# Performance work log

Measured on AMD Instinct MI355X. Metric: run time of the kernel, lower is better.

## Reference

```python
import jax, jax.numpy as jnp
import numpy as np

EPS = 1e-4  # scn BatchNormalization default eps
N, K, C = 500000, 9, 64  # active sites, kernel offsets (1x3x3), channels


def setup_inputs() -> dict:
    key = jax.random.key(0)
    ks = jax.random.split(key, 4)
    x = jax.random.normal(ks[0], (N, C), dtype=jnp.float32)
    nbr = jax.random.randint(ks[1], (N, K), 0, N)
    # submanifold conv: center offset maps each active site to itself
    nbr = nbr.at[:, K // 2].set(jnp.arange(N))
    scale = 1.0 / np.sqrt(K * C)
    w1 = jax.random.normal(ks[2], (K, C, C), dtype=jnp.float32) * scale
    w2 = jax.random.normal(ks[3], (K, C, C), dtype=jnp.float32) * scale
    gamma1 = jnp.ones((C,), jnp.float32)
    beta1 = jnp.zeros((C,), jnp.float32)
    gamma2 = jnp.ones((C,), jnp.float32)
    beta2 = jnp.zeros((C,), jnp.float32)
    return {"x": x, "nbr": nbr, "w1": w1, "w2": w2,
            "gamma1": gamma1, "beta1": beta1, "gamma2": gamma2, "beta2": beta2}


def _subm_conv(feats, nbr, w):
    # rulebook gather over active sites -> per-offset matmul -> accumulate
    g = feats[nbr]                              # [N, K, C]
    return jnp.einsum('nkc,kcd->nd', g, w)      # [N, C]


def _bn(feats, gamma, beta):
    # batch norm over all active sites (scn BatchNorm normalizes over rows)
    mu = jnp.mean(feats, axis=0)
    var = jnp.var(feats, axis=0)
    return (feats - mu) * jax.lax.rsqrt(var + EPS) * gamma + beta


def reference(x, nbr, w1, w2, gamma1, beta1, gamma2, beta2):
    out = _subm_conv(x, nbr, w1)                # conv1
    out = jax.nn.relu(_bn(out, gamma1, beta1))  # BatchNormReLU
    out = _subm_conv(out, nbr, w2)              # conv2
    out = _bn(out, gamma2, beta2)               # BatchNormalization
    return jax.nn.relu(out + x)                 # AddTable + ReLU
```

## Files before the change

### kernel.cpp

```cpp
#include <hip/hip_runtime.h>
#include <hip/hip_bf16.h>

typedef __attribute__((ext_vector_type(8))) short bf16x8;
typedef __attribute__((ext_vector_type(4))) float f32x4;

#define EPSV 1e-4f

static __device__ __forceinline__ unsigned short f2bf(float f) {
    unsigned int u = __builtin_bit_cast(unsigned int, f);
    u += 0x7FFFu + ((u >> 16) & 1u);
    return (unsigned short)(u >> 16);
}
static __device__ __forceinline__ float bf2f(unsigned short u) {
    unsigned int x = ((unsigned int)u) << 16;
    return __builtin_bit_cast(float, x);
}

__global__ __launch_bounds__(256) void k_cvt_bf16(
    const float* __restrict__ in, unsigned short* __restrict__ out, long n4) {
    long i0 = (long)blockIdx.x * 256 + threadIdx.x;
    long stride = (long)gridDim.x * 256;
    const float4* in4 = (const float4*)in;
    ushort4* out4 = (ushort4*)out;
    for (long i = i0; i < n4; i += stride) {
        float4 v = in4[i];
        ushort4 o;
        o.x = f2bf(v.x); o.y = f2bf(v.y); o.z = f2bf(v.z); o.w = f2bf(v.w);
        out4[i] = o;
    }
}

__global__ __launch_bounds__(256) void k_pack_w(
    const float* __restrict__ w, unsigned short* __restrict__ P) {
    int tid = blockIdx.x * 256 + threadIdx.x;
    if (tid >= 9 * 8 * 64) return;
    int lane = tid & 63;
    int f = tid >> 6;
    int t = f & 3, s = (f >> 2) & 1, k = f >> 3;
    int d = (t << 4) + (lane & 15);
    int c0 = (s << 5) + ((lane >> 4) << 3);
    bf16x8 v;
#pragma unroll
    for (int j = 0; j < 8; ++j)
        v[j] = (short)f2bf(w[((k * 64) + c0 + j) * 64 + d]);
    ((bf16x8*)P)[tid] = v;
}

__global__ __launch_bounds__(512, 4) void k_conv(
    const unsigned short* __restrict__ Xb,
    const int* __restrict__ nbr,
    const unsigned short* __restrict__ P,
    unsigned short* __restrict__ outb,
    float* __restrict__ partials,
    int n) {
    __shared__ unsigned short sB[36864];
    __shared__ float sStat[8][128];
    const int tid = threadIdx.x;
    const int w = tid >> 6, l = tid & 63;
    const int rl = l & 15, ch = l >> 4;
    const int bm = blockIdx.x * 256 + (w << 5);
    const bool valid = bm < n;
    const int r0 = valid ? bm + rl : 0;
    const int r1 = valid ? bm + 16 + rl : 0;

    {
        const float4* src = (const float4*)P;
        float4* dst = (float4*)sB;
#pragma unroll
        for (int i = 0; i < 9; ++i) dst[i * 512 + tid] = src[i * 512 + tid];
    }

    int idx0[9], idx1[9];
#pragma unroll
    for (int k = 0; k < 9; ++k) {
        idx0[k] = nbr[(long)r0 * 9 + k];
        idx1[k] = nbr[(long)r1 * 9 + k];
    }

    const bf16x8* __restrict__ Xv = (const bf16x8*)Xb;
    f32x4 acc0[4] = {}, acc1[4] = {};

    bf16x8 a[2][4];
    {
        long i0 = (long)idx0[0] * 8, i1 = (long)idx1[0] * 8;
        a[0][0] = Xv[i0 + ch];     a[0][1] = Xv[i0 + 4 + ch];
        a[0][2] = Xv[i1 + ch];     a[0][3] = Xv[i1 + 4 + ch];
        long j0 = (long)idx0[1] * 8, j1 = (long)idx1[1] * 8;
        a[1][0] = Xv[j0 + ch];     a[1][1] = Xv[j0 + 4 + ch];
        a[1][2] = Xv[j1 + ch];     a[1][3] = Xv[j1 + 4 + ch];
    }

    __syncthreads();

    const bf16x8* Bv = (const bf16x8*)sB;
#pragma unroll
    for (int k = 0; k < 9; ++k) {
        bf16x8 c0 = a[k & 1][0], c1 = a[k & 1][1];
        bf16x8 c2 = a[k & 1][2], c3 = a[k & 1][3];
        if (k < 7) {
            long j0 = (long)idx0[k + 2] * 8, j1 = (long)idx1[k + 2] * 8;
            a[k & 1][0] = Xv[j0 + ch];     a[k & 1][1] = Xv[j0 + 4 + ch];
            a[k & 1][2] = Xv[j1 + ch];     a[k & 1][3] = Xv[j1 + 4 + ch];
        }
#pragma unroll
        for (int t = 0; t < 4; ++t) {
            bf16x8 b0 = Bv[(k * 8 + t) * 64 + l];
            bf16x8 b1 = Bv[(k * 8 + 4 + t) * 64 + l];
            acc0[t] = __builtin_amdgcn_mfma_f32_16x16x32_bf16(c0, b0, acc0[t], 0, 0, 0);
            acc0[t] = __builtin_amdgcn_mfma_f32_16x16x32_bf16(c1, b1, acc0[t], 0, 0, 0);
            acc1[t] = __builtin_amdgcn_mfma_f32_16x16x32_bf16(c2, b0, acc1[t], 0, 0, 0);
            acc1[t] = __builtin_amdgcn_mfma_f32_16x16x32_bf16(c3, b1, acc1[t], 0, 0, 0);
        }
    }

    if (valid) {
#pragma unroll
        for (int t = 0; t < 4; ++t)
#pragma unroll
            for (int r = 0; r < 4; ++r) {
                outb[(long)(bm + (ch << 2) + r) * 64 + (t << 4) + rl] = f2bf(acc0[t][r]);
                outb[(long)(bm + 16 + (ch << 2) + r) * 64 + (t << 4) + rl] = f2bf(acc1[t][r]);
            }
    }

    float sa[4], sq[4];
#pragma unroll
    for (int t = 0; t < 4; ++t) {
        float s = 0.f, q = 0.f;
#pragma unroll
        for (int r = 0; r < 4; ++r) {
            s += acc0[t][r] + acc1[t][r];
            q += acc0[t][r] * acc0[t][r] + acc1[t][r] * acc1[t][r];
        }
        s += __shfl_xor(s, 16); s += __shfl_xor(s, 32);
        q += __shfl_xor(q, 16); q += __shfl_xor(q, 32);
        sa[t] = valid ? s : 0.f;
        sq[t] = valid ? q : 0.f;
    }
    if (l < 16) {
#pragma unroll
        for (int t = 0; t < 4; ++t) {
            sStat[w][(t << 4) + l] = sa[t];
            sStat[w][64 + (t << 4) + l] = sq[t];
        }
    }
    __syncthreads();
    if (tid < 128) {
        float s = 0.f;
#pragma unroll
        for (int i = 0; i < 8; ++i) s += sStat[i][tid];
        partials[(long)blockIdx.x * 128 + tid] = s;
    }
}

__global__ __launch_bounds__(256) void k_bnstats(
    const float* __restrict__ partials, int nb, int n,
    const float* __restrict__ gamma, const float* __restrict__ beta,
    float* __restrict__ ss) {
    const int d = blockIdx.x;
    const int tid = threadIdx.x;
    float s = 0.f, q = 0.f;
    for (int i = tid; i < nb; i += 256) {
        s += partials[(long)i * 128 + d];
        q += partials[(long)i * 128 + 64 + d];
    }
#pragma unroll
    for (int off = 32; off > 0; off >>= 1) {
        s += __shfl_xor(s, off);
        q += __shfl_xor(q, off);
    }
    __shared__ float rs_[4], rq_[4];
    if ((tid & 63) == 0) { rs_[tid >> 6] = s; rq_[tid >> 6] = q; }
    __syncthreads();
    if (tid == 0) {
        s = rs_[0] + rs_[1] + rs_[2] + rs_[3];
        q = rq_[0] + rq_[1] + rq_[2] + rq_[3];
        float mu = s / (float)n;
        float var = q / (float)n - mu * mu;
        float rsg = rsqrtf(var + EPSV);
        float sc = rsg * gamma[d];
        ss[d] = sc;
        ss[64 + d] = beta[d] - mu * sc;
    }
}

__global__ __launch_bounds__(256) void k_bnrelu(
    const unsigned short* __restrict__ in, const float* __restrict__ ss,
    unsigned short* __restrict__ outb, long n8) {
    __shared__ float ssc[64], ssh[64];
    if (threadIdx.x < 64) { ssc[threadIdx.x] = ss[threadIdx.x]; ssh[threadIdx.x] = ss[64 + threadIdx.x]; }
    __syncthreads();
    long i0 = (long)blockIdx.x * 256 + threadIdx.x;
    long stride = (long)gridDim.x * 256;
    const bf16x8* in8 = (const bf16x8*)in;
    bf16x8* o8 = (bf16x8*)outb;
    for (long i = i0; i < n8; i += stride) {
        bf16x8 v = in8[i];
        int db = (int)((i & 7) << 3);
        bf16x8 o;
#pragma unroll
        for (int j = 0; j < 8; ++j) {
            float f = bf2f((unsigned short)v[j]);
            f = fmaxf(f * ssc[db + j] + ssh[db + j], 0.f);
            o[j] = (short)f2bf(f);
        }
        o8[i] = o;
    }
}

__global__ __launch_bounds__(256) void k_final(
    float* __restrict__ out, const float* __restrict__ x,
    const unsigned short* __restrict__ c2, const float* __restrict__ ss, long n4) {
    __shared__ float ssc[64], ssh[64];
    if (threadIdx.x < 64) { ssc[threadIdx.x] = ss[threadIdx.x]; ssh[threadIdx.x] = ss[64 + threadIdx.x]; }
    __syncthreads();
    long i0 = (long)blockIdx.x * 256 + threadIdx.x;
    long stride = (long)gridDim.x * 256;
    const float4* x4 = (const float4*)x;
    const ushort4* c4 = (const ushort4*)c2;
    float4* o4 = (float4*)out;
    for (long i = i0; i < n4; i += stride) {
        ushort4 v = c4[i];
        float4 xv = x4[i];
        int db = (int)((i & 15) << 2);
        float4 r;
        r.x = fmaxf(bf2f(v.x) * ssc[db + 0] + ssh[db + 0] + xv.x, 0.f);
        r.y = fmaxf(bf2f(v.y) * ssc[db + 1] + ssh[db + 1] + xv.y, 0.f);
        r.z = fmaxf(bf2f(v.z) * ssc[db + 2] + ssh[db + 2] + xv.z, 0.f);
        r.w = fmaxf(bf2f(v.w) * ssc[db + 3] + ssh[db + 3] + xv.w, 0.f);
        o4[i] = r;
    }
}

extern "C" void kernel_launch(void* const* d_in, const int* in_sizes, int n_in,
                              void* d_out, int out_size, void* d_ws, size_t ws_size,
                              hipStream_t stream) {
    const float* x  = (const float*)d_in[0];
    const int* nbr  = (const int*)d_in[1];
    const float* w1 = (const float*)d_in[2];
    const float* w2 = (const float*)d_in[3];
    const float* g1 = (const float*)d_in[4];
    const float* b1 = (const float*)d_in[5];
    const float* g2 = (const float*)d_in[6];
    const float* b2 = (const float*)d_in[7];
    float* out = (float*)d_out;

    const int n = in_sizes[0] / 64;
    const int nbc = (n + 255) / 256;
    const long n64 = (long)n * 64;

    char* ws = (char*)d_ws;
    size_t off = 0;
    auto take = [&](size_t bytes) {
        char* p = ws + off;
        off = (off + bytes + 255) & ~(size_t)255;
        return p;
    };
    unsigned short* Xb    = (unsigned short*)take((size_t)n64 * 2);
    unsigned short* out1b = (unsigned short*)take((size_t)n64 * 2);
    float* partials       = (float*)take((size_t)nbc * 128 * 4);
    unsigned short* P1    = (unsigned short*)take(9 * 8192);
    unsigned short* P2    = (unsigned short*)take(9 * 8192);
    float* ss1            = (float*)take(128 * 4);
    float* ss2            = (float*)take(128 * 4);

    k_cvt_bf16<<<4096, 256, 0, stream>>>(x, Xb, n64 / 4);
    k_pack_w<<<18, 256, 0, stream>>>(w1, P1);
    k_pack_w<<<18, 256, 0, stream>>>(w2, P2);
    k_conv<<<nbc, 512, 0, stream>>>(Xb, nbr, P1, out1b, partials, n);
    k_bnstats<<<64, 256, 0, stream>>>(partials, nbc, n, g1, b1, ss1);
    k_bnrelu<<<2048, 256, 0, stream>>>(out1b, ss1, Xb, n64 / 8);
    k_conv<<<nbc, 512, 0, stream>>>(Xb, nbr, P2, out1b, partials, n);
    k_bnstats<<<64, 256, 0, stream>>>(partials, nbc, n, g2, b2, ss2);
    k_final<<<2048, 256, 0, stream>>>(out, x, out1b, ss2, n64 / 4);
}
```

Before: 316.9 us.

## Read conv weights from global, deepen gather prefetch, reuse bf16 residual

The conv kernel stops staging the packed weights in LDS and reads them straight from global/L2. This removes the 72KB shared buffer and the barrier, so more blocks can be resident. The gather prefetch now runs three offsets ahead instead of two, and the MFMA section gets a higher wave priority. The hidden activation is written into the output buffer as scratch so the bf16 copy of x survives, and the final kernel reads that bf16 residual instead of fp32 x. This halves the residual read but adds bf16 rounding error to the skip connection.

```diff
diff --git a/kernel.cpp b/kernel.cpp
--- a/kernel.cpp
+++ b/kernel.cpp
@@ -53,7 +53,6 @@
     unsigned short* __restrict__ outb,
     float* __restrict__ partials,
     int n) {
-    __shared__ unsigned short sB[36864];
     __shared__ float sStat[8][128];
     const int tid = threadIdx.x;
     const int w = tid >> 6, l = tid & 63;
@@ -63,13 +62,6 @@
     const int r0 = valid ? bm + rl : 0;
     const int r1 = valid ? bm + 16 + rl : 0;
 
-    {
-        const float4* src = (const float4*)P;
-        float4* dst = (float4*)sB;
-#pragma unroll
-        for (int i = 0; i < 9; ++i) dst[i * 512 + tid] = src[i * 512 + tid];
-    }
-
     int idx0[9], idx1[9];
 #pragma unroll
     for (int k = 0; k < 9; ++k) {
@@ -78,30 +70,28 @@
     }
 
     const bf16x8* __restrict__ Xv = (const bf16x8*)Xb;
+    const bf16x8* __restrict__ Bv = (const bf16x8*)P;
     f32x4 acc0[4] = {}, acc1[4] = {};
 
-    bf16x8 a[2][4];
-    {
-        long i0 = (long)idx0[0] * 8, i1 = (long)idx1[0] * 8;
-        a[0][0] = Xv[i0 + ch];     a[0][1] = Xv[i0 + 4 + ch];
-        a[0][2] = Xv[i1 + ch];     a[0][3] = Xv[i1 + 4 + ch];
-        long j0 = (long)idx0[1] * 8, j1 = (long)idx1[1] * 8;
-        a[1][0] = Xv[j0 + ch];     a[1][1] = Xv[j0 + 4 + ch];
-        a[1][2] = Xv[j1 + ch];     a[1][3] = Xv[j1 + 4 + ch];
-    }
-
-    __syncthreads();
-
-    const bf16x8* Bv = (const bf16x8*)sB;
+    bf16x8 a[3][4];
+#pragma unroll
+    for (int d = 0; d < 3; ++d) {
+        long i0 = (long)idx0[d] * 8, i1 = (long)idx1[d] * 8;
+        a[d][0] = Xv[i0 + ch];     a[d][1] = Xv[i0 + 4 + ch];
+        a[d][2] = Xv[i1 + ch];     a[d][3] = Xv[i1 + 4 + ch];
+    }
+
 #pragma unroll
     for (int k = 0; k < 9; ++k) {
-        bf16x8 c0 = a[k & 1][0], c1 = a[k & 1][1];
-        bf16x8 c2 = a[k & 1][2], c3 = a[k & 1][3];
-        if (k < 7) {
-            long j0 = (long)idx0[k + 2] * 8, j1 = (long)idx1[k + 2] * 8;
-            a[k & 1][0] = Xv[j0 + ch];     a[k & 1][1] = Xv[j0 + 4 + ch];
-            a[k & 1][2] = Xv[j1 + ch];     a[k & 1][3] = Xv[j1 + 4 + ch];
-        }
+        const int s = k % 3;
+        bf16x8 c0 = a[s][0], c1 = a[s][1];
+        bf16x8 c2 = a[s][2], c3 = a[s][3];
+        if (k < 6) {
+            long j0 = (long)idx0[k + 3] * 8, j1 = (long)idx1[k + 3] * 8;
+            a[s][0] = Xv[j0 + ch];     a[s][1] = Xv[j0 + 4 + ch];
+            a[s][2] = Xv[j1 + ch];     a[s][3] = Xv[j1 + 4 + ch];
+        }
+        __builtin_amdgcn_s_setprio(1);
 #pragma unroll
         for (int t = 0; t < 4; ++t) {
             bf16x8 b0 = Bv[(k * 8 + t) * 64 + l];
@@ -111,6 +101,7 @@
             acc1[t] = __builtin_amdgcn_mfma_f32_16x16x32_bf16(c2, b0, acc1[t], 0, 0, 0);
             acc1[t] = __builtin_amdgcn_mfma_f32_16x16x32_bf16(c3, b1, acc1[t], 0, 0, 0);
         }
+        __builtin_amdgcn_s_setprio(0);
     }
 
     if (valid) {
@@ -209,25 +200,25 @@
 }
 
 __global__ __launch_bounds__(256) void k_final(
-    float* __restrict__ out, const float* __restrict__ x,
+    float* __restrict__ out, const unsigned short* __restrict__ xb,
     const unsigned short* __restrict__ c2, const float* __restrict__ ss, long n4) {
     __shared__ float ssc[64], ssh[64];
     if (threadIdx.x < 64) { ssc[threadIdx.x] = ss[threadIdx.x]; ssh[threadIdx.x] = ss[64 + threadIdx.x]; }
     __syncthreads();
     long i0 = (long)blockIdx.x * 256 + threadIdx.x;
     long stride = (long)gridDim.x * 256;
-    const float4* x4 = (const float4*)x;
+    const ushort4* x4 = (const ushort4*)xb;
     const ushort4* c4 = (const ushort4*)c2;
     float4* o4 = (float4*)out;
     for (long i = i0; i < n4; i += stride) {
         ushort4 v = c4[i];
-        float4 xv = x4[i];
+        ushort4 xv = x4[i];
         int db = (int)((i & 15) << 2);
         float4 r;
-        r.x = fmaxf(bf2f(v.x) * ssc[db + 0] + ssh[db + 0] + xv.x, 0.f);
-        r.y = fmaxf(bf2f(v.y) * ssc[db + 1] + ssh[db + 1] + xv.y, 0.f);
-        r.z = fmaxf(bf2f(v.z) * ssc[db + 2] + ssh[db + 2] + xv.z, 0.f);
-        r.w = fmaxf(bf2f(v.w) * ssc[db + 3] + ssh[db + 3] + xv.w, 0.f);
+        r.x = fmaxf(bf2f(v.x) * ssc[db + 0] + ssh[db + 0] + bf2f(xv.x), 0.f);
+        r.y = fmaxf(bf2f(v.y) * ssc[db + 1] + ssh[db + 1] + bf2f(xv.y), 0.f);
+        r.z = fmaxf(bf2f(v.z) * ssc[db + 2] + ssh[db + 2] + bf2f(xv.z), 0.f);
+        r.w = fmaxf(bf2f(v.w) * ssc[db + 3] + ssh[db + 3] + bf2f(xv.w), 0.f);
         o4[i] = r;
     }
 }
@@ -263,14 +254,15 @@
     unsigned short* P2    = (unsigned short*)take(9 * 8192);
     float* ss1            = (float*)take(128 * 4);
     float* ss2            = (float*)take(128 * 4);
+    unsigned short* Hb    = (unsigned short*)d_out;
 
     k_cvt_bf16<<<4096, 256, 0, stream>>>(x, Xb, n64 / 4);
     k_pack_w<<<18, 256, 0, stream>>>(w1, P1);
     k_pack_w<<<18, 256, 0, stream>>>(w2, P2);
     k_conv<<<nbc, 512, 0, stream>>>(Xb, nbr, P1, out1b, partials, n);
     k_bnstats<<<64, 256, 0, stream>>>(partials, nbc, n, g1, b1, ss1);
-    k_bnrelu<<<2048, 256, 0, stream>>>(out1b, ss1, Xb, n64 / 8);
-    k_conv<<<nbc, 512, 0, stream>>>(Xb, nbr, P2, out1b, partials, n);
+    k_bnrelu<<<2048, 256, 0, stream>>>(out1b, ss1, Hb, n64 / 8);
+    k_conv<<<nbc, 512, 0, stream>>>(Hb, nbr, P2, out1b, partials, n);
     k_bnstats<<<64, 256, 0, stream>>>(partials, nbc, n, g2, b2, ss2);
-    k_final<<<2048, 256, 0, stream>>>(out, x, out1b, ss2, n64 / 4);
-}
+    k_final<<<2048, 256, 0, stream>>>(out, Xb, out1b, ss2, n64 / 4);
+}
```

New measurement: 376.7 us. +18.9%, slower.
